# Performance work log

Hardware: AMD Instinct MI355X
Metric: run time of the kernel (lower is better)

The kernel has to match this reference:

```python
import jax, jax.numpy as jnp
import numpy as np

B, S, D, H = 2, 2048, 1024, 16
DK = D // H  # 64


def setup_inputs() -> dict:
    rng = jax.random.key(0)
    ks = jax.random.split(rng, 11)
    std = 1.0 / np.sqrt(D)
    query = jax.random.normal(ks[0], (B, S, D), dtype=jnp.float32)
    key = jax.random.normal(ks[1], (B, S, D), dtype=jnp.float32)
    value = jax.random.normal(ks[2], (B, S, D), dtype=jnp.float32)
    # causal mask, broadcast over batch and heads
    mask = jnp.tril(jnp.ones((S, S), dtype=jnp.int32))[None, None]
    Wq = jax.random.normal(ks[3], (D, D), dtype=jnp.float32) * std
    bq = jnp.zeros((D,), dtype=jnp.float32)
    Wk = jax.random.normal(ks[4], (D, D), dtype=jnp.float32) * std
    bk = jnp.zeros((D,), dtype=jnp.float32)
    Wv = jax.random.normal(ks[5], (D, D), dtype=jnp.float32) * std
    bv = jnp.zeros((D,), dtype=jnp.float32)
    Wo = jax.random.normal(ks[6], (D, D), dtype=jnp.float32) * std
    bo = jnp.zeros((D,), dtype=jnp.float32)
    return {"query": query, "key": key, "value": value, "mask": mask,
            "Wq": Wq, "bq": bq, "Wk": Wk, "bk": bk,
            "Wv": Wv, "bv": bv, "Wo": Wo, "bo": bo}


def reference(query, key, value, mask, Wq, bq, Wk, bk, Wv, bv, Wo, bo):
    scale = jnp.sqrt(jnp.float32(DK))
    # linear projections (nn.Linear applies x @ W.T + b)
    Q = query @ Wq.T + bq
    K = key @ Wk.T + bk
    V = value @ Wv.T + bv
    # [B,S,D] -> [B,H,S,DK]
    Q = Q.reshape(B, S, H, DK).transpose(0, 2, 1, 3)
    K = K.reshape(B, S, H, DK).transpose(0, 2, 1, 3)
    V = V.reshape(B, S, H, DK).transpose(0, 2, 1, 3)
    scores = jnp.einsum('bhqd,bhkd->bhqk', Q, K) / scale
    scores = jnp.where(mask == 0, jnp.float32(-1e9), scores)
    attention = jax.nn.softmax(scores, axis=-1)  # dropout is identity in eval
    x = jnp.einsum('bhqk,bhkd->bhqd', attention, V)
    x = x.transpose(0, 2, 1, 3).reshape(B, S, D)
    x = x @ Wo.T + bo
    return (x, attention)
```

## Files before the change

kernel.cpp:

```cpp
#include <hip/hip_runtime.h>
#include <stdint.h>

#define S_LEN 2048
#define DMODEL 1024
#define NHEAD 16
#define DKH 64
#define NROW 4096

using short8  = __attribute__((ext_vector_type(8))) short;
using short4v = __attribute__((ext_vector_type(4))) short;
using float4v = __attribute__((ext_vector_type(4))) float;

__device__ __forceinline__ short f2bf(float f) {
    union { float f; unsigned u; } v; v.f = f;
    unsigned r = (v.u + 0x7fffu + ((v.u >> 16) & 1u)) >> 16;
    return (short)r;
}

__device__ __forceinline__ float bf2f(short b) {
    union { unsigned u; float f; } c;
    c.u = ((unsigned)(unsigned short)b) << 16;
    return c.f;
}

__device__ __forceinline__ float4v mfma16(short8 a, short8 b, float4v c) {
    return __builtin_amdgcn_mfma_f32_16x16x32_bf16(a, b, c, 0, 0, 0);
}

__device__ __forceinline__ void gload16(const short* g, short* l) {
    __builtin_amdgcn_global_load_lds(
        (const __attribute__((address_space(1))) void*)g,
        (__attribute__((address_space(3))) void*)l, 16, 0, 0);
}

__global__ __launch_bounds__(256) void convert_kernel(
    const float* __restrict__ q, const float* __restrict__ k, const float* __restrict__ v,
    const float* __restrict__ wq, const float* __restrict__ wk, const float* __restrict__ wv,
    const float* __restrict__ wo,
    short* __restrict__ oq, short* __restrict__ ok_, short* __restrict__ ov,
    short* __restrict__ owq, short* __restrict__ owk, short* __restrict__ owv,
    short* __restrict__ owo)
{
    const size_t A = (size_t)NROW * DMODEL;
    const size_t W = (size_t)DMODEL * DMODEL;
    size_t i = ((size_t)blockIdx.x * 256 + threadIdx.x) * 4;
    const float* src; short* dst; size_t off;
    if (i < A)            { src = q;  dst = oq;  off = i; }
    else if (i < 2 * A)   { src = k;  dst = ok_; off = i - A; }
    else if (i < 3 * A)   { src = v;  dst = ov;  off = i - 2 * A; }
    else {
        size_t j = i - 3 * A; int wsel = (int)(j / W); off = j % W;
        src = (wsel == 0) ? wq : (wsel == 1) ? wk : (wsel == 2) ? wv : wo;
        dst = (wsel == 0) ? owq : (wsel == 1) ? owk : (wsel == 2) ? owv : owo;
    }
    float4v x = *(const float4v*)(src + off);
    short4v o;
    o[0] = f2bf(x[0]); o[1] = f2bf(x[1]); o[2] = f2bf(x[2]); o[3] = f2bf(x[3]);
    *(short4v*)(dst + off) = o;
}

__global__ __launch_bounds__(256) void gemm_qkv(
    const short* __restrict__ Xq, const short* __restrict__ Xk, const short* __restrict__ Xv,
    const short* __restrict__ Wq, const short* __restrict__ Wk, const short* __restrict__ Wv,
    const float* __restrict__ bq, const float* __restrict__ bk, const float* __restrict__ bv,
    short* __restrict__ Qo, short* __restrict__ Ko, short* __restrict__ Vt)
{
    int zy = blockIdx.y;
    int z = zy >> 3;
    int n0 = (zy & 7) * 128;
    const short* X = (z == 0) ? Xq : (z == 1) ? Xk : Xv;
    const short* W = (z == 0) ? Wq : (z == 1) ? Wk : Wv;
    const float* bias = (z == 0) ? bq : (z == 1) ? bk : bv;
    int m0 = blockIdx.x * 128;

    __shared__ __align__(16) short As[128 * 32];
    __shared__ __align__(16) short Bs[128 * 32];

    int tid = threadIdx.x, lane = tid & 63, w = tid >> 6;
    int row_in = lane & 15, grp = lane >> 4;
    int wm = (w & 1) * 64, wn = (w >> 1) * 64;

    float4v acc[4][4];
#pragma unroll
    for (int m = 0; m < 4; m++)
#pragma unroll
        for (int n = 0; n < 4; n++) acc[m][n] = (float4v){0.f, 0.f, 0.f, 0.f};

    for (int k0 = 0; k0 < DMODEL; k0 += 32) {
#pragma unroll
        for (int j = 0; j < 2; j++) {
            int chunk = j * 256 + tid;
            int r = chunk >> 2, c = (chunk & 3) * 8;
            gload16(X + (size_t)(m0 + r) * DMODEL + k0 + c,
                    As + (size_t)(j * 256 + w * 64) * 8);
            gload16(W + (size_t)(n0 + r) * DMODEL + k0 + c,
                    Bs + (size_t)(j * 256 + w * 64) * 8);
        }
        __syncthreads();

        short8 af[4], bf[4];
#pragma unroll
        for (int m = 0; m < 4; m++)
            af[m] = *(const short8*)&As[(wm + m * 16 + row_in) * 32 + grp * 8];
#pragma unroll
        for (int n = 0; n < 4; n++)
            bf[n] = *(const short8*)&Bs[(wn + n * 16 + row_in) * 32 + grp * 8];
#pragma unroll
        for (int m = 0; m < 4; m++)
#pragma unroll
            for (int n = 0; n < 4; n++)
                acc[m][n] = mfma16(af[m], bf[n], acc[m][n]);
        __syncthreads();
    }

#pragma unroll
    for (int m = 0; m < 4; m++) {
#pragma unroll
        for (int n = 0; n < 4; n++) {
            int col = n0 + wn + n * 16 + row_in;
            int h = col >> 6, dk = col & 63;
            float bval = bias[col];
            if (z < 2) {
                short* dst = (z == 0) ? Qo : Ko;
#pragma unroll
                for (int r = 0; r < 4; r++) {
                    int rowg = m0 + wm + m * 16 + grp * 4 + r;
                    int bb = rowg >> 11, s = rowg & 2047;
                    dst[(((size_t)(bb * NHEAD + h)) * S_LEN + s) * DKH + dk] =
                        f2bf(acc[m][n][r] + bval);
                }
            } else {
                int rowg0 = m0 + wm + m * 16 + grp * 4;
                int bb = rowg0 >> 11, s0 = rowg0 & 2047;
                short4v pk;
#pragma unroll
                for (int r = 0; r < 4; r++) pk[r] = f2bf(acc[m][n][r] + bval);
                *(short4v*)(Vt + ((size_t)(bb * NHEAD + h) * DKH + dk) * S_LEN + s0) = pk;
            }
        }
    }
}

__global__ __launch_bounds__(256) void gemm_out(
    const short* __restrict__ X, const short* __restrict__ W,
    const float* __restrict__ bias, float* __restrict__ out)
{
    int m0 = blockIdx.x * 128, n0 = blockIdx.y * 128;

    __shared__ __align__(16) short As[128 * 32];
    __shared__ __align__(16) short Bs[128 * 32];

    int tid = threadIdx.x, lane = tid & 63, w = tid >> 6;
    int row_in = lane & 15, grp = lane >> 4;
    int wm = (w & 1) * 64, wn = (w >> 1) * 64;

    float4v acc[4][4];
#pragma unroll
    for (int m = 0; m < 4; m++)
#pragma unroll
        for (int n = 0; n < 4; n++) acc[m][n] = (float4v){0.f, 0.f, 0.f, 0.f};

    for (int k0 = 0; k0 < DMODEL; k0 += 32) {
#pragma unroll
        for (int j = 0; j < 2; j++) {
            int chunk = j * 256 + tid;
            int r = chunk >> 2, c = (chunk & 3) * 8;
            gload16(X + (size_t)(m0 + r) * DMODEL + k0 + c,
                    As + (size_t)(j * 256 + w * 64) * 8);
            gload16(W + (size_t)(n0 + r) * DMODEL + k0 + c,
                    Bs + (size_t)(j * 256 + w * 64) * 8);
        }
        __syncthreads();

        short8 af[4], bf[4];
#pragma unroll
        for (int m = 0; m < 4; m++)
            af[m] = *(const short8*)&As[(wm + m * 16 + row_in) * 32 + grp * 8];
#pragma unroll
        for (int n = 0; n < 4; n++)
            bf[n] = *(const short8*)&Bs[(wn + n * 16 + row_in) * 32 + grp * 8];
#pragma unroll
        for (int m = 0; m < 4; m++)
#pragma unroll
            for (int n = 0; n < 4; n++)
                acc[m][n] = mfma16(af[m], bf[n], acc[m][n]);
        __syncthreads();
    }

#pragma unroll
    for (int m = 0; m < 4; m++)
#pragma unroll
        for (int n = 0; n < 4; n++) {
            int col = n0 + wn + n * 16 + row_in;
            float bval = bias[col];
#pragma unroll
            for (int r = 0; r < 4; r++) {
                int rowg = m0 + wm + m * 16 + grp * 4 + r;
                out[(size_t)rowg * DMODEL + col] = acc[m][n][r] + bval;
            }
        }
}

__global__ __launch_bounds__(256) void attn_kernel(
    const short* __restrict__ Q, const short* __restrict__ K, const short* __restrict__ Vt,
    float* __restrict__ Attn, short* __restrict__ Xatt)
{
    int bh = blockIdx.x;
    int q0 = blockIdx.y * 64;
    int tid = threadIdx.x, lane = tid & 63, w = tid >> 6;
    int row_in = lane & 15, grp = lane >> 4;
    int qbase = q0 + w * 16;

    const short* Qh = Q + (size_t)bh * S_LEN * DKH;
    const short* Kh = K + (size_t)bh * S_LEN * DKH;
    const short* Vh = Vt + (size_t)bh * DKH * S_LEN;
    float* Ah = Attn + (size_t)bh * S_LEN * S_LEN;

    __shared__ __align__(16) short Ks[64 * 72];
    __shared__ __align__(16) short Vs[64 * 72];
    __shared__ __align__(16) short Plds[4][16 * 72];

    short8 qf0 = *(const short8*)(Qh + (size_t)(qbase + row_in) * DKH + grp * 8);
    short8 qf1 = *(const short8*)(Qh + (size_t)(qbase + row_in) * DKH + 32 + grp * 8);

    const float SC = 0.125f * 1.44269504f;
    float l[4] = {0.f, 0.f, 0.f, 0.f};
    int Tmax = q0 / 64 + 1;

    for (int t = 0; t < Tmax; t++) {
        int kv0 = t * 64;
        {
            const short* src = Kh + (size_t)kv0 * DKH;
#pragma unroll
            for (int j = 0; j < 2; j++) {
                int ch = j * 256 + tid;
                int r = ch >> 3, c = (ch & 7) * 8;
                short8 kv = *(const short8*)(src + ch * 8);
                *(short8*)&Ks[r * 72 + c] = kv;
            }
        }
        __syncthreads();
#pragma unroll
        for (int u = 0; u < 4; u++) {
            short8 b0 = *(const short8*)&Ks[(u * 16 + row_in) * 72 + grp * 8];
            short8 b1 = *(const short8*)&Ks[(u * 16 + row_in) * 72 + 32 + grp * 8];
            float4v a = (float4v){0.f, 0.f, 0.f, 0.f};
            a = mfma16(qf0, b0, a);
            a = mfma16(qf1, b1, a);
            int colg = kv0 + u * 16 + row_in;
#pragma unroll
            for (int r = 0; r < 4; r++) {
                int rowg = qbase + grp * 4 + r;
                float e = (colg > rowg) ? 0.0f : exp2f(a[r] * SC);
                l[r] += e;
            }
        }
        __syncthreads();
    }
    float rinv[4];
#pragma unroll
    for (int r = 0; r < 4; r++) {
        float s = l[r];
        s += __shfl_xor(s, 1, 64);
        s += __shfl_xor(s, 2, 64);
        s += __shfl_xor(s, 4, 64);
        s += __shfl_xor(s, 8, 64);
        rinv[r] = 1.0f / s;
    }

    float4v o[4];
#pragma unroll
    for (int v = 0; v < 4; v++) o[v] = (float4v){0.f, 0.f, 0.f, 0.f};

    for (int t = 0; t < Tmax; t++) {
        int kv0 = t * 64;
        {
            const short* srcK = Kh + (size_t)kv0 * DKH;
#pragma unroll
            for (int j = 0; j < 2; j++) {
                int ch = j * 256 + tid;
                int r = ch >> 3, c = (ch & 7) * 8;
                short8 kv = *(const short8*)(srcK + ch * 8);
                *(short8*)&Ks[r * 72 + c] = kv;
                short8 vv = *(const short8*)(Vh + (size_t)r * S_LEN + kv0 + c);
                *(short8*)&Vs[r * 72 + c] = vv;
            }
        }
        __syncthreads();
#pragma unroll
        for (int u = 0; u < 4; u++) {
            short8 b0 = *(const short8*)&Ks[(u * 16 + row_in) * 72 + grp * 8];
            short8 b1 = *(const short8*)&Ks[(u * 16 + row_in) * 72 + 32 + grp * 8];
            float4v a = (float4v){0.f, 0.f, 0.f, 0.f};
            a = mfma16(qf0, b0, a);
            a = mfma16(qf1, b1, a);
            int colg = kv0 + u * 16 + row_in;
#pragma unroll
            for (int r = 0; r < 4; r++) {
                int rowg = qbase + grp * 4 + r;
                float p = (colg > rowg) ? 0.0f : exp2f(a[r] * SC) * rinv[r];
                Plds[w][(grp * 4 + r) * 72 + u * 16 + row_in] = f2bf(p);
            }
        }
        asm volatile("s_waitcnt lgkmcnt(0)" ::: "memory");
#pragma unroll
        for (int rr = 0; rr < 4; rr++) {
            int rloc = rr * 4 + grp;
            short4v pb = *(const short4v*)&Plds[w][rloc * 72 + row_in * 4];
            float4v pf;
#pragma unroll
            for (int i = 0; i < 4; i++) pf[i] = bf2f(pb[i]);
            *(float4v*)(Ah + (size_t)(qbase + rloc) * S_LEN + kv0 + row_in * 4) = pf;
        }
        short8 pa0 = *(const short8*)&Plds[w][row_in * 72 + grp * 8];
        short8 pa1 = *(const short8*)&Plds[w][row_in * 72 + 32 + grp * 8];
#pragma unroll
        for (int v = 0; v < 4; v++) {
            short8 b0 = *(const short8*)&Vs[(v * 16 + row_in) * 72 + grp * 8];
            short8 b1 = *(const short8*)&Vs[(v * 16 + row_in) * 72 + 32 + grp * 8];
            o[v] = mfma16(pa0, b0, o[v]);
            o[v] = mfma16(pa1, b1, o[v]);
        }
        __syncthreads();
    }

    float4v zz = (float4v){0.f, 0.f, 0.f, 0.f};
    for (int kv0 = Tmax * 64; kv0 < S_LEN; kv0 += 64) {
#pragma unroll
        for (int r = 0; r < 4; r++) {
            int rowg = qbase + r * 4 + grp;
            *(float4v*)(Ah + (size_t)rowg * S_LEN + kv0 + row_in * 4) = zz;
        }
    }

    int b = bh >> 4, h = bh & 15;
#pragma unroll
    for (int v = 0; v < 4; v++) {
#pragma unroll
        for (int r = 0; r < 4; r++) {
            int s = qbase + grp * 4 + r;
            int col = h * 64 + v * 16 + row_in;
            Xatt[(size_t)(b * S_LEN + s) * DMODEL + col] = f2bf(o[v][r]);
        }
    }
}

extern "C" void kernel_launch(void* const* d_in, const int* in_sizes, int n_in,
                              void* d_out, int out_size, void* d_ws, size_t ws_size,
                              hipStream_t stream) {
    const float* q  = (const float*)d_in[0];
    const float* k  = (const float*)d_in[1];
    const float* v  = (const float*)d_in[2];
    const float* Wq = (const float*)d_in[4];
    const float* bq = (const float*)d_in[5];
    const float* Wk = (const float*)d_in[6];
    const float* bk = (const float*)d_in[7];
    const float* Wv = (const float*)d_in[8];
    const float* bv = (const float*)d_in[9];
    const float* Wo = (const float*)d_in[10];
    const float* bo = (const float*)d_in[11];

    float* out_x    = (float*)d_out;
    float* out_attn = out_x + (size_t)NROW * DMODEL;

    char* ws = (char*)d_ws;
    size_t off = 0;
    auto carve = [&](size_t bytes) -> char* {
        char* p = ws + off;
        off += (bytes + 255) & ~(size_t)255;
        return p;
    };
    const size_t XB = (size_t)NROW * DMODEL * sizeof(short);
    const size_t WB = (size_t)DMODEL * DMODEL * sizeof(short);
    short* Xq  = (short*)carve(XB);
    short* Xk  = (short*)carve(XB);
    short* Xv  = (short*)carve(XB);
    short* Wqb = (short*)carve(WB);
    short* Wkb = (short*)carve(WB);
    short* Wvb = (short*)carve(WB);
    short* Wob = (short*)carve(WB);
    short* Qb  = (short*)carve(XB);
    short* Kb  = (short*)carve(XB);
    short* Vtb = (short*)carve(XB);
    short* Xat = (short*)carve(XB);

    convert_kernel<<<dim3(16384), dim3(256), 0, stream>>>(
        q, k, v, Wq, Wk, Wv, Wo, Xq, Xk, Xv, Wqb, Wkb, Wvb, Wob);

    gemm_qkv<<<dim3(NROW / 128, 24), dim3(256), 0, stream>>>(
        Xq, Xk, Xv, Wqb, Wkb, Wvb, bq, bk, bv, Qb, Kb, Vtb);

    attn_kernel<<<dim3(32, S_LEN / 64), dim3(256), 0, stream>>>(
        Qb, Kb, Vtb, out_attn, Xat);

    gemm_out<<<dim3(NROW / 128, DMODEL / 128), dim3(256), 0, stream>>>(
        Xat, Wob, bo, out_x);
}
```

Baseline: 731.4 us.

## Replace two-pass softmax with single pass and deferred normalization via bf16 scratch

The first pass that computed the softmax row sums is removed. Unnormalized exp values are written as bf16 to a workspace buffer while PV is accumulated, and the output is scaled by 1/l at the end. A final sweep rereads the bf16 scratch, normalizes it and writes the fp32 attention matrix, and tiles are now scheduled heaviest-first by reversing the query-block order. This saves the QK^T recompute and half the K loads, at the cost of an extra 256MB bf16 write and reread in the workspace; it uses no running max, so it relies on the scores being small enough that exp2 does not overflow.

```diff
diff --git a/kernel.cpp b/kernel.cpp
--- a/kernel.cpp
+++ b/kernel.cpp
@@ -203,10 +203,10 @@
 
 __global__ __launch_bounds__(256) void attn_kernel(
     const short* __restrict__ Q, const short* __restrict__ K, const short* __restrict__ Vt,
-    float* __restrict__ Attn, short* __restrict__ Xatt)
+    short* __restrict__ Pws, float* __restrict__ Attn, short* __restrict__ Xatt)
 {
     int bh = blockIdx.x;
-    int q0 = blockIdx.y * 64;
+    int q0 = (int)(gridDim.y - 1 - blockIdx.y) * 64;
     int tid = threadIdx.x, lane = tid & 63, w = tid >> 6;
     int row_in = lane & 15, grp = lane >> 4;
     int qbase = q0 + w * 16;
@@ -214,63 +214,23 @@
     const short* Qh = Q + (size_t)bh * S_LEN * DKH;
     const short* Kh = K + (size_t)bh * S_LEN * DKH;
     const short* Vh = Vt + (size_t)bh * DKH * S_LEN;
+    short* Ph = Pws + (size_t)bh * S_LEN * S_LEN;
     float* Ah = Attn + (size_t)bh * S_LEN * S_LEN;
 
     __shared__ __align__(16) short Ks[64 * 72];
     __shared__ __align__(16) short Vs[64 * 72];
     __shared__ __align__(16) short Plds[4][16 * 72];
+    __shared__ float rinv_s[64];
 
     short8 qf0 = *(const short8*)(Qh + (size_t)(qbase + row_in) * DKH + grp * 8);
     short8 qf1 = *(const short8*)(Qh + (size_t)(qbase + row_in) * DKH + 32 + grp * 8);
 
     const float SC = 0.125f * 1.44269504f;
     float l[4] = {0.f, 0.f, 0.f, 0.f};
+    float4v o[4];
+#pragma unroll
+    for (int v = 0; v < 4; v++) o[v] = (float4v){0.f, 0.f, 0.f, 0.f};
     int Tmax = q0 / 64 + 1;
-
-    for (int t = 0; t < Tmax; t++) {
-        int kv0 = t * 64;
-        {
-            const short* src = Kh + (size_t)kv0 * DKH;
-#pragma unroll
-            for (int j = 0; j < 2; j++) {
-                int ch = j * 256 + tid;
-                int r = ch >> 3, c = (ch & 7) * 8;
-                short8 kv = *(const short8*)(src + ch * 8);
-                *(short8*)&Ks[r * 72 + c] = kv;
-            }
-        }
-        __syncthreads();
-#pragma unroll
-        for (int u = 0; u < 4; u++) {
-            short8 b0 = *(const short8*)&Ks[(u * 16 + row_in) * 72 + grp * 8];
-            short8 b1 = *(const short8*)&Ks[(u * 16 + row_in) * 72 + 32 + grp * 8];
-            float4v a = (float4v){0.f, 0.f, 0.f, 0.f};
-            a = mfma16(qf0, b0, a);
-            a = mfma16(qf1, b1, a);
-            int colg = kv0 + u * 16 + row_in;
-#pragma unroll
-            for (int r = 0; r < 4; r++) {
-                int rowg = qbase + grp * 4 + r;
-                float e = (colg > rowg) ? 0.0f : exp2f(a[r] * SC);
-                l[r] += e;
-            }
-        }
-        __syncthreads();
-    }
-    float rinv[4];
-#pragma unroll
-    for (int r = 0; r < 4; r++) {
-        float s = l[r];
-        s += __shfl_xor(s, 1, 64);
-        s += __shfl_xor(s, 2, 64);
-        s += __shfl_xor(s, 4, 64);
-        s += __shfl_xor(s, 8, 64);
-        rinv[r] = 1.0f / s;
-    }
-
-    float4v o[4];
-#pragma unroll
-    for (int v = 0; v < 4; v++) o[v] = (float4v){0.f, 0.f, 0.f, 0.f};
 
     for (int t = 0; t < Tmax; t++) {
         int kv0 = t * 64;
@@ -298,20 +258,12 @@
 #pragma unroll
             for (int r = 0; r < 4; r++) {
                 int rowg = qbase + grp * 4 + r;
-                float p = (colg > rowg) ? 0.0f : exp2f(a[r] * SC) * rinv[r];
-                Plds[w][(grp * 4 + r) * 72 + u * 16 + row_in] = f2bf(p);
+                float e = (colg > rowg) ? 0.0f : exp2f(a[r] * SC);
+                l[r] += e;
+                Plds[w][(grp * 4 + r) * 72 + u * 16 + row_in] = f2bf(e);
             }
         }
         asm volatile("s_waitcnt lgkmcnt(0)" ::: "memory");
-#pragma unroll
-        for (int rr = 0; rr < 4; rr++) {
-            int rloc = rr * 4 + grp;
-            short4v pb = *(const short4v*)&Plds[w][rloc * 72 + row_in * 4];
-            float4v pf;
-#pragma unroll
-            for (int i = 0; i < 4; i++) pf[i] = bf2f(pb[i]);
-            *(float4v*)(Ah + (size_t)(qbase + rloc) * S_LEN + kv0 + row_in * 4) = pf;
-        }
         short8 pa0 = *(const short8*)&Plds[w][row_in * 72 + grp * 8];
         short8 pa1 = *(const short8*)&Plds[w][row_in * 72 + 32 + grp * 8];
 #pragma unroll
@@ -321,16 +273,29 @@
             o[v] = mfma16(pa0, b0, o[v]);
             o[v] = mfma16(pa1, b1, o[v]);
         }
-        __syncthreads();
-    }
-
-    float4v zz = (float4v){0.f, 0.f, 0.f, 0.f};
-    for (int kv0 = Tmax * 64; kv0 < S_LEN; kv0 += 64) {
-#pragma unroll
-        for (int r = 0; r < 4; r++) {
-            int rowg = qbase + r * 4 + grp;
-            *(float4v*)(Ah + (size_t)rowg * S_LEN + kv0 + row_in * 4) = zz;
-        }
+#pragma unroll
+        for (int rr = 0; rr < 2; rr++) {
+            int rloc = rr * 8 + (lane >> 3);
+            int c8 = (lane & 7) * 8;
+            short8 pb = *(const short8*)&Plds[w][rloc * 72 + c8];
+            *(short8*)(Ph + (size_t)(qbase + rloc) * S_LEN + kv0 + c8) = pb;
+        }
+        __syncthreads();
+    }
+
+    float rinv[4];
+#pragma unroll
+    for (int r = 0; r < 4; r++) {
+        float s = l[r];
+        s += __shfl_xor(s, 1, 64);
+        s += __shfl_xor(s, 2, 64);
+        s += __shfl_xor(s, 4, 64);
+        s += __shfl_xor(s, 8, 64);
+        rinv[r] = 1.0f / s;
+    }
+    if (row_in == 0) {
+#pragma unroll
+        for (int r = 0; r < 4; r++) rinv_s[w * 16 + grp * 4 + r] = rinv[r];
     }
 
     int b = bh >> 4, h = bh & 15;
@@ -340,8 +305,40 @@
         for (int r = 0; r < 4; r++) {
             int s = qbase + grp * 4 + r;
             int col = h * 64 + v * 16 + row_in;
-            Xatt[(size_t)(b * S_LEN + s) * DMODEL + col] = f2bf(o[v][r]);
-        }
+            Xatt[(size_t)(b * S_LEN + s) * DMODEL + col] = f2bf(o[v][r] * rinv[r]);
+        }
+    }
+    __syncthreads();
+
+    int rB = tid >> 2;
+    int cB = (tid & 3) * 16;
+    float rv = rinv_s[rB];
+    const short* prow = Ph + (size_t)(q0 + rB) * S_LEN;
+    float* arow = Ah + (size_t)(q0 + rB) * S_LEN;
+    int kvEnd = Tmax * 64;
+    for (int kv0 = 0; kv0 < kvEnd; kv0 += 64) {
+        short8 p0 = *(const short8*)(prow + kv0 + cB);
+        short8 p1 = *(const short8*)(prow + kv0 + cB + 8);
+        float4v f0, f1, f2, f3;
+#pragma unroll
+        for (int i = 0; i < 4; i++) f0[i] = bf2f(p0[i]) * rv;
+#pragma unroll
+        for (int i = 0; i < 4; i++) f1[i] = bf2f(p0[i + 4]) * rv;
+#pragma unroll
+        for (int i = 0; i < 4; i++) f2[i] = bf2f(p1[i]) * rv;
+#pragma unroll
+        for (int i = 0; i < 4; i++) f3[i] = bf2f(p1[i + 4]) * rv;
+        *(float4v*)(arow + kv0 + cB)      = f0;
+        *(float4v*)(arow + kv0 + cB + 4)  = f1;
+        *(float4v*)(arow + kv0 + cB + 8)  = f2;
+        *(float4v*)(arow + kv0 + cB + 12) = f3;
+    }
+    float4v zz = (float4v){0.f, 0.f, 0.f, 0.f};
+    for (int kv0 = kvEnd; kv0 < S_LEN; kv0 += 64) {
+        *(float4v*)(arow + kv0 + cB)      = zz;
+        *(float4v*)(arow + kv0 + cB + 4)  = zz;
+        *(float4v*)(arow + kv0 + cB + 8)  = zz;
+        *(float4v*)(arow + kv0 + cB + 12) = zz;
     }
 }
 
@@ -372,6 +369,7 @@
     };
     const size_t XB = (size_t)NROW * DMODEL * sizeof(short);
     const size_t WB = (size_t)DMODEL * DMODEL * sizeof(short);
+    const size_t PB = (size_t)2 * NHEAD * S_LEN * S_LEN * sizeof(short);
     short* Xq  = (short*)carve(XB);
     short* Xk  = (short*)carve(XB);
     short* Xv  = (short*)carve(XB);
@@ -383,6 +381,7 @@
     short* Kb  = (short*)carve(XB);
     short* Vtb = (short*)carve(XB);
     short* Xat = (short*)carve(XB);
+    short* Pws = (short*)carve(PB);
 
     convert_kernel<<<dim3(16384), dim3(256), 0, stream>>>(
         q, k, v, Wq, Wk, Wv, Wo, Xq, Xk, Xv, Wqb, Wkb, Wvb, Wob);
@@ -391,7 +390,7 @@
         Xq, Xk, Xv, Wqb, Wkb, Wvb, bq, bk, bv, Qb, Kb, Vtb);
 
     attn_kernel<<<dim3(32, S_LEN / 64), dim3(256), 0, stream>>>(
-        Qb, Kb, Vtb, out_attn, Xat);
+        Qb, Kb, Vtb, Pws, out_attn, Xat);
 
     gemm_out<<<dim3(NROW / 128, DMODEL / 128), dim3(256), 0, stream>>>(
         Xat, Wob, bo, out_x);
```

Result: slower. 862.1 us (+17.9%).

## Cache unnormalized probabilities in workspace instead of recomputing QK^T in second pass

Applied to the files above, without the earlier changes.

The first pass now writes the unnormalized bf16 exp scores to a 256MB global workspace. The second pass reads them back, scales them by the row reciprocal when writing the attention output, and feeds them directly to the PV MFMA. Normalization of the output is deferred to the final store. Query tiles are also launched in reverse order so the longest causal blocks start first. This removes the second QK^T MFMA, the exp and the K reload, at the cost of a large extra global write and read of P, which may become memory-bound.

```diff
diff --git a/kernel.cpp b/kernel.cpp
--- a/kernel.cpp
+++ b/kernel.cpp
@@ -203,10 +203,10 @@
 
 __global__ __launch_bounds__(256) void attn_kernel(
     const short* __restrict__ Q, const short* __restrict__ K, const short* __restrict__ Vt,
-    float* __restrict__ Attn, short* __restrict__ Xatt)
+    short* __restrict__ Pws, float* __restrict__ Attn, short* __restrict__ Xatt)
 {
     int bh = blockIdx.x;
-    int q0 = blockIdx.y * 64;
+    int q0 = (int)(gridDim.y - 1 - blockIdx.y) * 64;
     int tid = threadIdx.x, lane = tid & 63, w = tid >> 6;
     int row_in = lane & 15, grp = lane >> 4;
     int qbase = q0 + w * 16;
@@ -214,11 +214,12 @@
     const short* Qh = Q + (size_t)bh * S_LEN * DKH;
     const short* Kh = K + (size_t)bh * S_LEN * DKH;
     const short* Vh = Vt + (size_t)bh * DKH * S_LEN;
+    short* Ph = Pws + (size_t)bh * S_LEN * S_LEN;
     float* Ah = Attn + (size_t)bh * S_LEN * S_LEN;
 
     __shared__ __align__(16) short Ks[64 * 72];
-    __shared__ __align__(16) short Vs[64 * 72];
-    __shared__ __align__(16) short Plds[4][16 * 72];
+    __shared__ __align__(16) short VP[64 * 72];
+    __shared__ float rinv_s[64];
 
     short8 qf0 = *(const short8*)(Qh + (size_t)(qbase + row_in) * DKH + grp * 8);
     short8 qf1 = *(const short8*)(Qh + (size_t)(qbase + row_in) * DKH + 32 + grp * 8);
@@ -230,12 +231,12 @@
     for (int t = 0; t < Tmax; t++) {
         int kv0 = t * 64;
         {
-            const short* src = Kh + (size_t)kv0 * DKH;
+            const short* srcK = Kh + (size_t)kv0 * DKH;
 #pragma unroll
             for (int j = 0; j < 2; j++) {
                 int ch = j * 256 + tid;
                 int r = ch >> 3, c = (ch & 7) * 8;
-                short8 kv = *(const short8*)(src + ch * 8);
+                short8 kv = *(const short8*)(srcK + ch * 8);
                 *(short8*)&Ks[r * 72 + c] = kv;
             }
         }
@@ -253,10 +254,20 @@
                 int rowg = qbase + grp * 4 + r;
                 float e = (colg > rowg) ? 0.0f : exp2f(a[r] * SC);
                 l[r] += e;
+                VP[w * 1152 + (grp * 4 + r) * 72 + u * 16 + row_in] = f2bf(e);
             }
         }
-        __syncthreads();
-    }
+        asm volatile("s_waitcnt lgkmcnt(0)" ::: "memory");
+#pragma unroll
+        for (int rr = 0; rr < 2; rr++) {
+            int rloc = rr * 8 + (lane >> 3);
+            int c8 = (lane & 7) * 8;
+            short8 pb = *(const short8*)&VP[w * 1152 + rloc * 72 + c8];
+            *(short8*)(Ph + (size_t)(qbase + rloc) * S_LEN + kv0 + c8) = pb;
+        }
+        __syncthreads();
+    }
+
     float rinv[4];
 #pragma unroll
     for (int r = 0; r < 4; r++) {
@@ -267,61 +278,55 @@
         s += __shfl_xor(s, 8, 64);
         rinv[r] = 1.0f / s;
     }
+    if (row_in == 0) {
+#pragma unroll
+        for (int r = 0; r < 4; r++) rinv_s[w * 16 + grp * 4 + r] = rinv[r];
+    }
 
     float4v o[4];
 #pragma unroll
     for (int v = 0; v < 4; v++) o[v] = (float4v){0.f, 0.f, 0.f, 0.f};
+
+    short8 pa0 = *(const short8*)(Ph + (size_t)(qbase + row_in) * S_LEN + grp * 8);
+    short8 pa1 = *(const short8*)(Ph + (size_t)(qbase + row_in) * S_LEN + 32 + grp * 8);
 
     for (int t = 0; t < Tmax; t++) {
         int kv0 = t * 64;
         {
-            const short* srcK = Kh + (size_t)kv0 * DKH;
 #pragma unroll
             for (int j = 0; j < 2; j++) {
                 int ch = j * 256 + tid;
                 int r = ch >> 3, c = (ch & 7) * 8;
-                short8 kv = *(const short8*)(srcK + ch * 8);
-                *(short8*)&Ks[r * 72 + c] = kv;
                 short8 vv = *(const short8*)(Vh + (size_t)r * S_LEN + kv0 + c);
-                *(short8*)&Vs[r * 72 + c] = vv;
+                *(short8*)&VP[r * 72 + c] = vv;
             }
         }
         __syncthreads();
-#pragma unroll
-        for (int u = 0; u < 4; u++) {
-            short8 b0 = *(const short8*)&Ks[(u * 16 + row_in) * 72 + grp * 8];
-            short8 b1 = *(const short8*)&Ks[(u * 16 + row_in) * 72 + 32 + grp * 8];
-            float4v a = (float4v){0.f, 0.f, 0.f, 0.f};
-            a = mfma16(qf0, b0, a);
-            a = mfma16(qf1, b1, a);
-            int colg = kv0 + u * 16 + row_in;
-#pragma unroll
-            for (int r = 0; r < 4; r++) {
-                int rowg = qbase + grp * 4 + r;
-                float p = (colg > rowg) ? 0.0f : exp2f(a[r] * SC) * rinv[r];
-                Plds[w][(grp * 4 + r) * 72 + u * 16 + row_in] = f2bf(p);
-            }
-        }
-        asm volatile("s_waitcnt lgkmcnt(0)" ::: "memory");
+        short8 na0 = pa0, na1 = pa1;
+        if (t + 1 < Tmax) {
+            int kv1 = kv0 + 64;
+            na0 = *(const short8*)(Ph + (size_t)(qbase + row_in) * S_LEN + kv1 + grp * 8);
+            na1 = *(const short8*)(Ph + (size_t)(qbase + row_in) * S_LEN + kv1 + 32 + grp * 8);
+        }
 #pragma unroll
         for (int rr = 0; rr < 4; rr++) {
             int rloc = rr * 4 + grp;
-            short4v pb = *(const short4v*)&Plds[w][rloc * 72 + row_in * 4];
+            float rv = rinv_s[w * 16 + rloc];
+            short4v pb = *(const short4v*)(Ph + (size_t)(qbase + rloc) * S_LEN + kv0 + row_in * 4);
             float4v pf;
 #pragma unroll
-            for (int i = 0; i < 4; i++) pf[i] = bf2f(pb[i]);
+            for (int i = 0; i < 4; i++) pf[i] = bf2f(pb[i]) * rv;
             *(float4v*)(Ah + (size_t)(qbase + rloc) * S_LEN + kv0 + row_in * 4) = pf;
         }
-        short8 pa0 = *(const short8*)&Plds[w][row_in * 72 + grp * 8];
-        short8 pa1 = *(const short8*)&Plds[w][row_in * 72 + 32 + grp * 8];
 #pragma unroll
         for (int v = 0; v < 4; v++) {
-            short8 b0 = *(const short8*)&Vs[(v * 16 + row_in) * 72 + grp * 8];
-            short8 b1 = *(const short8*)&Vs[(v * 16 + row_in) * 72 + 32 + grp * 8];
+            short8 b0 = *(const short8*)&VP[(v * 16 + row_in) * 72 + grp * 8];
+            short8 b1 = *(const short8*)&VP[(v * 16 + row_in) * 72 + 32 + grp * 8];
             o[v] = mfma16(pa0, b0, o[v]);
             o[v] = mfma16(pa1, b1, o[v]);
         }
         __syncthreads();
+        pa0 = na0; pa1 = na1;
     }
 
     float4v zz = (float4v){0.f, 0.f, 0.f, 0.f};
@@ -340,7 +345,7 @@
         for (int r = 0; r < 4; r++) {
             int s = qbase + grp * 4 + r;
             int col = h * 64 + v * 16 + row_in;
-            Xatt[(size_t)(b * S_LEN + s) * DMODEL + col] = f2bf(o[v][r]);
+            Xatt[(size_t)(b * S_LEN + s) * DMODEL + col] = f2bf(o[v][r] * rinv[r]);
         }
     }
 }
@@ -372,6 +377,7 @@
     };
     const size_t XB = (size_t)NROW * DMODEL * sizeof(short);
     const size_t WB = (size_t)DMODEL * DMODEL * sizeof(short);
+    const size_t PB = (size_t)2 * NHEAD * S_LEN * S_LEN * sizeof(short);
     short* Xq  = (short*)carve(XB);
     short* Xk  = (short*)carve(XB);
     short* Xv  = (short*)carve(XB);
@@ -383,6 +389,7 @@
     short* Kb  = (short*)carve(XB);
     short* Vtb = (short*)carve(XB);
     short* Xat = (short*)carve(XB);
+    short* Pws = (short*)carve(PB);
 
     convert_kernel<<<dim3(16384), dim3(256), 0, stream>>>(
         q, k, v, Wq, Wk, Wv, Wo, Xq, Xk, Xv, Wqb, Wkb, Wvb, Wob);
@@ -391,7 +398,7 @@
         Xq, Xk, Xv, Wqb, Wkb, Wvb, bq, bk, bv, Qb, Kb, Vtb);
 
     attn_kernel<<<dim3(32, S_LEN / 64), dim3(256), 0, stream>>>(
-        Qb, Kb, Vtb, out_attn, Xat);
+        Qb, Kb, Vtb, Pws, out_attn, Xat);
 
     gemm_out<<<dim3(NROW / 128, DMODEL / 128), dim3(256), 0, stream>>>(
         Xat, Wob, bo, out_x);
```

After: 809.7 us. 1.11x slower.

## Split attention into single-pass PV kernel and separate column-wise probability writer

Applied to the files above, without the earlier changes.

The attention kernel no longer does a separate row-sum pass. It accumulates unnormalized exp values and the row sum in one pass, normalizes the output at the end, and saves 1/sum per row to a workspace buffer. A new kernel, launched after the output GEMM, recomputes QK^T per key tile across all query tiles and writes the normalized probabilities and the zero upper triangle. Attention blocks are also launched in reverse order so the heaviest query tiles start first. This removes the duplicated QK^T pass and the slow fp32 attention-matrix stores from the main kernel, at the cost of recomputing scores and adding an extra launch. The probabilities are now written directly from fp32 instead of being rounded through bf16. Neither version subtracts the row max before exponentiating.

```diff
diff --git a/kernel.cpp b/kernel.cpp
--- a/kernel.cpp
+++ b/kernel.cpp
@@ -203,10 +203,10 @@
 
 __global__ __launch_bounds__(256) void attn_kernel(
     const short* __restrict__ Q, const short* __restrict__ K, const short* __restrict__ Vt,
-    float* __restrict__ Attn, short* __restrict__ Xatt)
+    float* __restrict__ rinvg, short* __restrict__ Xatt)
 {
     int bh = blockIdx.x;
-    int q0 = blockIdx.y * 64;
+    int q0 = (int)(gridDim.y - 1 - blockIdx.y) * 64;
     int tid = threadIdx.x, lane = tid & 63, w = tid >> 6;
     int row_in = lane & 15, grp = lane >> 4;
     int qbase = q0 + w * 16;
@@ -214,7 +214,6 @@
     const short* Qh = Q + (size_t)bh * S_LEN * DKH;
     const short* Kh = K + (size_t)bh * S_LEN * DKH;
     const short* Vh = Vt + (size_t)bh * DKH * S_LEN;
-    float* Ah = Attn + (size_t)bh * S_LEN * S_LEN;
 
     __shared__ __align__(16) short Ks[64 * 72];
     __shared__ __align__(16) short Vs[64 * 72];
@@ -225,52 +224,10 @@
 
     const float SC = 0.125f * 1.44269504f;
     float l[4] = {0.f, 0.f, 0.f, 0.f};
+    float4v o[4];
+#pragma unroll
+    for (int v = 0; v < 4; v++) o[v] = (float4v){0.f, 0.f, 0.f, 0.f};
     int Tmax = q0 / 64 + 1;
-
-    for (int t = 0; t < Tmax; t++) {
-        int kv0 = t * 64;
-        {
-            const short* src = Kh + (size_t)kv0 * DKH;
-#pragma unroll
-            for (int j = 0; j < 2; j++) {
-                int ch = j * 256 + tid;
-                int r = ch >> 3, c = (ch & 7) * 8;
-                short8 kv = *(const short8*)(src + ch * 8);
-                *(short8*)&Ks[r * 72 + c] = kv;
-            }
-        }
-        __syncthreads();
-#pragma unroll
-        for (int u = 0; u < 4; u++) {
-            short8 b0 = *(const short8*)&Ks[(u * 16 + row_in) * 72 + grp * 8];
-            short8 b1 = *(const short8*)&Ks[(u * 16 + row_in) * 72 + 32 + grp * 8];
-            float4v a = (float4v){0.f, 0.f, 0.f, 0.f};
-            a = mfma16(qf0, b0, a);
-            a = mfma16(qf1, b1, a);
-            int colg = kv0 + u * 16 + row_in;
-#pragma unroll
-            for (int r = 0; r < 4; r++) {
-                int rowg = qbase + grp * 4 + r;
-                float e = (colg > rowg) ? 0.0f : exp2f(a[r] * SC);
-                l[r] += e;
-            }
-        }
-        __syncthreads();
-    }
-    float rinv[4];
-#pragma unroll
-    for (int r = 0; r < 4; r++) {
-        float s = l[r];
-        s += __shfl_xor(s, 1, 64);
-        s += __shfl_xor(s, 2, 64);
-        s += __shfl_xor(s, 4, 64);
-        s += __shfl_xor(s, 8, 64);
-        rinv[r] = 1.0f / s;
-    }
-
-    float4v o[4];
-#pragma unroll
-    for (int v = 0; v < 4; v++) o[v] = (float4v){0.f, 0.f, 0.f, 0.f};
 
     for (int t = 0; t < Tmax; t++) {
         int kv0 = t * 64;
@@ -298,20 +255,12 @@
 #pragma unroll
             for (int r = 0; r < 4; r++) {
                 int rowg = qbase + grp * 4 + r;
-                float p = (colg > rowg) ? 0.0f : exp2f(a[r] * SC) * rinv[r];
-                Plds[w][(grp * 4 + r) * 72 + u * 16 + row_in] = f2bf(p);
+                float e = (colg > rowg) ? 0.0f : exp2f(a[r] * SC);
+                l[r] += e;
+                Plds[w][(grp * 4 + r) * 72 + u * 16 + row_in] = f2bf(e);
             }
         }
         asm volatile("s_waitcnt lgkmcnt(0)" ::: "memory");
-#pragma unroll
-        for (int rr = 0; rr < 4; rr++) {
-            int rloc = rr * 4 + grp;
-            short4v pb = *(const short4v*)&Plds[w][rloc * 72 + row_in * 4];
-            float4v pf;
-#pragma unroll
-            for (int i = 0; i < 4; i++) pf[i] = bf2f(pb[i]);
-            *(float4v*)(Ah + (size_t)(qbase + rloc) * S_LEN + kv0 + row_in * 4) = pf;
-        }
         short8 pa0 = *(const short8*)&Plds[w][row_in * 72 + grp * 8];
         short8 pa1 = *(const short8*)&Plds[w][row_in * 72 + 32 + grp * 8];
 #pragma unroll
@@ -324,13 +273,20 @@
         __syncthreads();
     }
 
-    float4v zz = (float4v){0.f, 0.f, 0.f, 0.f};
-    for (int kv0 = Tmax * 64; kv0 < S_LEN; kv0 += 64) {
-#pragma unroll
-        for (int r = 0; r < 4; r++) {
-            int rowg = qbase + r * 4 + grp;
-            *(float4v*)(Ah + (size_t)rowg * S_LEN + kv0 + row_in * 4) = zz;
-        }
+    float rinv[4];
+#pragma unroll
+    for (int r = 0; r < 4; r++) {
+        float s = l[r];
+        s += __shfl_xor(s, 1, 64);
+        s += __shfl_xor(s, 2, 64);
+        s += __shfl_xor(s, 4, 64);
+        s += __shfl_xor(s, 8, 64);
+        rinv[r] = 1.0f / s;
+    }
+    if (row_in == 0) {
+#pragma unroll
+        for (int r = 0; r < 4; r++)
+            rinvg[(size_t)bh * S_LEN + qbase + grp * 4 + r] = rinv[r];
     }
 
     int b = bh >> 4, h = bh & 15;
@@ -340,8 +296,86 @@
         for (int r = 0; r < 4; r++) {
             int s = qbase + grp * 4 + r;
             int col = h * 64 + v * 16 + row_in;
-            Xatt[(size_t)(b * S_LEN + s) * DMODEL + col] = f2bf(o[v][r]);
-        }
+            Xatt[(size_t)(b * S_LEN + s) * DMODEL + col] = f2bf(o[v][r] * rinv[r]);
+        }
+    }
+}
+
+__global__ __launch_bounds__(256) void attn_write_kernel(
+    const short* __restrict__ Q, const short* __restrict__ K,
+    const float* __restrict__ rinvg, float* __restrict__ Attn)
+{
+    int bh = blockIdx.x;
+    int t  = blockIdx.y;
+    int kv0 = t * 64;
+    int tid = threadIdx.x, lane = tid & 63, w = tid >> 6;
+    int row_in = lane & 15, grp = lane >> 4;
+
+    const short* Qh = Q + (size_t)bh * S_LEN * DKH;
+    const short* Kh = K + (size_t)bh * S_LEN * DKH;
+    const float* rh = rinvg + (size_t)bh * S_LEN;
+    float* Ah = Attn + (size_t)bh * S_LEN * S_LEN;
+
+    __shared__ __align__(16) short Ks[64 * 72];
+    {
+        const short* srcK = Kh + (size_t)kv0 * DKH;
+#pragma unroll
+        for (int j = 0; j < 2; j++) {
+            int ch = j * 256 + tid;
+            int r = ch >> 3, c = (ch & 7) * 8;
+            *(short8*)&Ks[r * 72 + c] = *(const short8*)(srcK + ch * 8);
+        }
+    }
+    __syncthreads();
+
+    short8 kb0[4], kb1[4];
+#pragma unroll
+    for (int u = 0; u < 4; u++) {
+        kb0[u] = *(const short8*)&Ks[(u * 16 + row_in) * 72 + grp * 8];
+        kb1[u] = *(const short8*)&Ks[(u * 16 + row_in) * 72 + 32 + grp * 8];
+    }
+
+    float4v zz = (float4v){0.f, 0.f, 0.f, 0.f};
+    for (int s = 0; s < t; s++) {
+        float* base = Ah + (size_t)(s * 64) * S_LEN + kv0;
+#pragma unroll
+        for (int kk = 0; kk < 4; kk++) {
+            int idx = kk * 256 + tid;
+            int r = idx >> 4, c = (idx & 15) * 4;
+            *(float4v*)(base + (size_t)r * S_LEN + c) = zz;
+        }
+    }
+
+    const float SC = 0.125f * 1.44269504f;
+    int qb = t * 64 + w * 16;
+    short8 qf0 = *(const short8*)(Qh + (size_t)(qb + row_in) * DKH + grp * 8);
+    short8 qf1 = *(const short8*)(Qh + (size_t)(qb + row_in) * DKH + 32 + grp * 8);
+
+    for (int s = t; s < 32; s++) {
+        int qbase = s * 64 + w * 16;
+        short8 nq0 = qf0, nq1 = qf1;
+        if (s + 1 < 32) {
+            int nqb = (s + 1) * 64 + w * 16;
+            nq0 = *(const short8*)(Qh + (size_t)(nqb + row_in) * DKH + grp * 8);
+            nq1 = *(const short8*)(Qh + (size_t)(nqb + row_in) * DKH + 32 + grp * 8);
+        }
+        float rv[4];
+#pragma unroll
+        for (int r = 0; r < 4; r++) rv[r] = rh[qbase + grp * 4 + r];
+#pragma unroll
+        for (int u = 0; u < 4; u++) {
+            float4v a = (float4v){0.f, 0.f, 0.f, 0.f};
+            a = mfma16(qf0, kb0[u], a);
+            a = mfma16(qf1, kb1[u], a);
+            int colg = kv0 + u * 16 + row_in;
+#pragma unroll
+            for (int r = 0; r < 4; r++) {
+                int rowg = qbase + grp * 4 + r;
+                float p = (colg > rowg) ? 0.0f : exp2f(a[r] * SC) * rv[r];
+                Ah[(size_t)rowg * S_LEN + colg] = p;
+            }
+        }
+        qf0 = nq0; qf1 = nq1;
     }
 }
 
@@ -383,6 +417,7 @@
     short* Kb  = (short*)carve(XB);
     short* Vtb = (short*)carve(XB);
     short* Xat = (short*)carve(XB);
+    float* Rin = (float*)carve((size_t)2 * NHEAD * S_LEN * sizeof(float));
 
     convert_kernel<<<dim3(16384), dim3(256), 0, stream>>>(
         q, k, v, Wq, Wk, Wv, Wo, Xq, Xk, Xv, Wqb, Wkb, Wvb, Wob);
@@ -391,8 +426,11 @@
         Xq, Xk, Xv, Wqb, Wkb, Wvb, bq, bk, bv, Qb, Kb, Vtb);
 
     attn_kernel<<<dim3(32, S_LEN / 64), dim3(256), 0, stream>>>(
-        Qb, Kb, Vtb, out_attn, Xat);
+        Qb, Kb, Vtb, Rin, Xat);
 
     gemm_out<<<dim3(NROW / 128, DMODEL / 128), dim3(256), 0, stream>>>(
         Xat, Wob, bo, out_x);
-}
+
+    attn_write_kernel<<<dim3(32, 32), dim3(256), 0, stream>>>(
+        Qb, Kb, Rin, out_attn);
+}
```

New measurement: 788.0 us. 1.08x slower.
